# Performance work log

Measured on AMD Instinct MI355X. Metric: run time of the kernel, lower is better.

## Reference

```python
import jax, jax.numpy as jnp
import numpy as np

V, E, H, S, B = 32000, 512, 512, 512, 32  # vocab, emb=n_unit, hidden, srclen, batch


def _lstm_zero_state_step(x, W_ih, b_ih, b_hh):
    """PyTorch LSTM single step with zero initial (h, c).
    With h0 = 0, the recurrent term h0 @ W_hh^T vanishes, so W_hh does not
    affect the output (faithful to the original, which never passes state).
    Gate order i, f, g, o. Works on [..., in_dim] batched inputs.
    """
    gates = x @ W_ih.T + b_ih + b_hh
    i, f, g, o = jnp.split(gates, 4, axis=-1)
    c = jax.nn.sigmoid(i) * jnp.tanh(g)  # f gate multiplies c0 = 0
    h = jax.nn.sigmoid(o) * jnp.tanh(c)
    return h, c


def setup_inputs() -> dict:
    key = jax.random.key(0)
    ks = jax.random.split(key, 10)
    s = 1.0 / np.sqrt(H)
    return {
        "src_seqs": jax.random.randint(ks[0], (S, B), 0, V),
        "W_emb": jax.random.normal(ks[1], (V, E), dtype=jnp.float32) * 0.02,
        # read LSTM (E -> H)
        "W_ih_r": jax.random.uniform(ks[2], (4 * H, E), minval=-s, maxval=s),
        "b_ih_r": jax.random.uniform(ks[3], (4 * H,), minval=-s, maxval=s),
        "b_hh_r": jax.random.uniform(ks[4], (4 * H,), minval=-s, maxval=s),
        # compose MLP (2H -> 2H)
        "W_c": jax.random.uniform(ks[5], (2 * H, 2 * H), minval=-s, maxval=s),
        "b_c": jax.random.uniform(ks[6], (2 * H,), minval=-s, maxval=s),
        # write LSTM (2H -> H)
        "W_ih_w": jax.random.uniform(ks[7], (4 * H, 2 * H), minval=-s, maxval=s),
        "b_ih_w": jax.random.uniform(ks[8], (4 * H,), minval=-s, maxval=s),
        "b_hh_w": jax.random.uniform(ks[9], (4 * H,), minval=-s, maxval=s),
    }


def reference(src_seqs, W_emb, W_ih_r, b_ih_r, b_hh_r, W_c, b_c,
              W_ih_w, b_ih_w, b_hh_w):
    emb = W_emb[src_seqs]                     # [S, B, E]
    # read LSTM is stateless per step (zero init state each call) -> vectorize
    o_all, _ = _lstm_zero_state_step(emb, W_ih_r, b_ih_r, b_hh_r)  # [S, B, H]
    M0 = jnp.transpose(emb, (1, 0, 2))        # [B, S, H] memory

    def step(M, o_t):
        # read: attention over memory
        z = jax.nn.softmax(jnp.einsum('bsh,bh->bs', M, o_t), axis=1)  # [B, S]
        m = jnp.einsum('bs,bsh->bh', z, M)                            # [B, H]
        # compose
        c_in = jnp.concatenate([o_t, m], axis=1) @ W_c.T + b_c        # [B, 2H]
        # write LSTM (also stateless per call)
        h, cell = _lstm_zero_state_step(c_in, W_ih_w, b_ih_w, b_hh_w)  # [B, H]
        # erase/write memory update
        M_new = (1.0 - z)[..., None] * M + z[..., None] * h[:, None, :]
        return M_new, (h, cell)

    _, (hs, cells) = jax.lax.scan(step, M0, o_all)
    outputs = hs                              # [S, B, H]
    h_n = hs[-1][None]                        # [1, B, H] (n_layer=1)
    c_n = cells[-1][None]                     # [1, B, H]
    return outputs, h_n, c_n
```

## Files before the change

### kernel.cpp

```cpp
#include <hip/hip_runtime.h>
#include <hip/hip_bf16.h>

#define S_LEN 512
#define B_SZ  32
#define H_DIM 512
#define KC    1024

typedef __attribute__((ext_vector_type(8)))  short  short8;
typedef __attribute__((ext_vector_type(4)))  float  f32x4;
typedef __attribute__((ext_vector_type(2)))  float  f32x2;

static __device__ __forceinline__ unsigned short f2bf(float f){
  unsigned u = __float_as_uint(f);
  u += 0x7fffu + ((u >> 16) & 1u);
  return (unsigned short)(u >> 16);
}
static __device__ __forceinline__ short8 cvt8(float4 a, float4 b){
  short8 r;
  r[0]=(short)f2bf(a.x); r[1]=(short)f2bf(a.y); r[2]=(short)f2bf(a.z); r[3]=(short)f2bf(a.w);
  r[4]=(short)f2bf(b.x); r[5]=(short)f2bf(b.y); r[6]=(short)f2bf(b.z); r[7]=(short)f2bf(b.w);
  return r;
}
static __device__ __forceinline__ short8 cvt8e(f32x4 a, f32x4 b){
  short8 r;
  r[0]=(short)f2bf(a[0]); r[1]=(short)f2bf(a[1]); r[2]=(short)f2bf(a[2]); r[3]=(short)f2bf(a[3]);
  r[4]=(short)f2bf(b[0]); r[5]=(short)f2bf(b[1]); r[6]=(short)f2bf(b[2]); r[7]=(short)f2bf(b[3]);
  return r;
}
static __device__ __forceinline__ float sigf(float x){ return 1.0f/(1.0f+__expf(-x)); }
static __device__ __forceinline__ float tanh_(float x){
  float e = __expf(2.0f*x);
  return (e-1.0f)/(e+1.0f);
}

static __device__ __forceinline__ void st_ag(float* p, float v){
  __hip_atomic_store(p, v, __ATOMIC_RELAXED, __HIP_MEMORY_SCOPE_AGENT);
}
static __device__ __forceinline__ f32x2 ld2_ag(const float* p){
  unsigned long long u = __hip_atomic_load((unsigned long long*)p, __ATOMIC_RELAXED, __HIP_MEMORY_SCOPE_AGENT);
  f32x2 r; r[0] = __uint_as_float((unsigned)u); r[1] = __uint_as_float((unsigned)(u>>32));
  return r;
}

__global__ __launch_bounds__(256) void k_gather_emb(const int* __restrict__ src,
    const float* __restrict__ Wemb, unsigned short* __restrict__ embB){
  int gid = blockIdx.x*256 + threadIdx.x;
  int row = gid >> 6;
  int k   = (gid & 63) * 8;
  int idx = src[row];
  const float* p = Wemb + (size_t)idx*H_DIM + k;
  float4 a = *(const float4*)p;
  float4 b = *(const float4*)(p+4);
  *(short8*)(embB + (size_t)gid*8) = cvt8(a,b);
}

__global__ __launch_bounds__(256) void k_perm_wr(const float* __restrict__ W,
    unsigned short* __restrict__ out){
  int gid = blockIdx.x*256 + threadIdx.x;
  int n = gid >> 6;
  int k = (gid & 63)*8;
  int j = (n&3)*512 + (n>>2);
  const float* p = W + (size_t)j*512 + k;
  float4 a = *(const float4*)p;
  float4 b = *(const float4*)(p+4);
  *(short8*)(out + (size_t)gid*8) = cvt8(a,b);
}

__global__ __launch_bounds__(256) void k_perm_wihw(const float* __restrict__ W,
    unsigned short* __restrict__ out){
  int gid = blockIdx.x*256 + threadIdx.x;
  int n = gid >> 7;
  int k = (gid & 127)*8;
  int j = (n&3)*512 + (n>>2);
  const float* p = W + (size_t)j*KC + k;
  float4 a = *(const float4*)p;
  float4 b = *(const float4*)(p+4);
  *(short8*)(out + (size_t)gid*8) = cvt8(a,b);
}

__global__ __launch_bounds__(256) void k_wcT(const float* __restrict__ Wc,
    unsigned short* __restrict__ out){
  __shared__ float tile[64][65];
  int bx = blockIdx.x & 15, by = blockIdx.x >> 4;
  int c0 = bx*64, r0 = by*64;
  int row = threadIdx.x >> 2;
  int cp  = (threadIdx.x & 3)*16;
  for (int i=0;i<16;i+=4){
    float4 v = *(const float4*)&Wc[(size_t)(r0+row)*KC + c0 + cp + i];
    tile[row][cp+i+0]=v.x; tile[row][cp+i+1]=v.y; tile[row][cp+i+2]=v.z; tile[row][cp+i+3]=v.w;
  }
  __syncthreads();
  short8 s0, s1;
  for(int i=0;i<8;++i){
    s0[i]=(short)f2bf(tile[cp+i][row]);
    s1[i]=(short)f2bf(tile[cp+8+i][row]);
  }
  unsigned short* op = out + (size_t)(c0+row)*KC + r0 + cp;
  *(short8*)op = s0; *(short8*)(op+8) = s1;
}

__global__ __launch_bounds__(256) void k_bias_r(const float* __restrict__ bi,
    const float* __restrict__ bh, float* __restrict__ out){
  int n = blockIdx.x*256 + threadIdx.x;
  int j = (n&3)*512 + (n>>2);
  out[n] = bi[j] + bh[j];
}

__global__ __launch_bounds__(256) void k_bcomb(const float* __restrict__ Wihw,
    const float* __restrict__ bc, const float* __restrict__ bi,
    const float* __restrict__ bh, float* __restrict__ out){
  int n = blockIdx.x*256 + threadIdx.x;
  int j = (n&3)*512 + (n>>2);
  const float* wp = Wihw + (size_t)j*KC;
  float s = 0.f;
  for (int l=0;l<KC;l+=4){
    float4 w = *(const float4*)&wp[l];
    float4 c = *(const float4*)&bc[l];
    s += w.x*c.x + w.y*c.y + w.z*c.z + w.w*c.w;
  }
  out[n] = s + bi[j] + bh[j];
}

template<int EPI>
__global__ __launch_bounds__(256) void gemm_k(const unsigned short* __restrict__ A,
    const unsigned short* __restrict__ Bm, int K, int bnCnt,
    const float* __restrict__ bias, float* __restrict__ outF,
    unsigned short* __restrict__ outB, int outStride){
  __shared__ __align__(16) char smem[66560];
  unsigned short* As = (unsigned short*)smem;
  unsigned short* Bs = As + 128*72;
  float* epi = (float*)smem;
  const int tid = threadIdx.x, lane = tid & 63, w = tid >> 6;
  const int wr = w >> 1, wc = w & 1;
  const int bm = blockIdx.x / bnCnt, bn = blockIdx.x % bnCnt;
  f32x4 acc[4][4] = {};
  const size_t Abase = (size_t)bm*128*K;
  const size_t Bbase = (size_t)bn*128*K;
  for (int k0 = 0; k0 < K; k0 += 64){
    __syncthreads();
    #pragma unroll
    for (int i = 0; i < 4; ++i){
      int idx = tid + i*256;
      int row = idx >> 3, cb = (idx & 7)*8;
      *(short8*)&As[row*72 + cb] = *(const short8*)&A[Abase + (size_t)row*K + k0 + cb];
      *(short8*)&Bs[row*72 + cb] = *(const short8*)&Bm[Bbase + (size_t)row*K + k0 + cb];
    }
    __syncthreads();
    #pragma unroll
    for (int kk = 0; kk < 64; kk += 32){
      short8 af[4], bf[4];
      #pragma unroll
      for (int i=0;i<4;++i) af[i] = *(short8*)&As[(wr*64 + i*16 + (lane&15))*72 + kk + (lane>>4)*8];
      #pragma unroll
      for (int j=0;j<4;++j) bf[j] = *(short8*)&Bs[(wc*64 + j*16 + (lane&15))*72 + kk + (lane>>4)*8];
      #pragma unroll
      for (int i=0;i<4;++i)
        #pragma unroll
        for (int j=0;j<4;++j)
          acc[i][j] = __builtin_amdgcn_mfma_f32_16x16x32_bf16(af[i], bf[j], acc[i][j], 0,0,0);
    }
  }
  if (EPI == 0){
    float bj[4];
    #pragma unroll
    for (int j=0;j<4;++j) bj[j] = bias[bn*128 + wc*64 + j*16 + (lane&15)];
    __syncthreads();
    float* ep = epi + w*(64*65);
    #pragma unroll
    for (int i=0;i<4;++i)
      #pragma unroll
      for (int j=0;j<4;++j)
        #pragma unroll
        for (int r=0;r<4;++r)
          ep[(i*16 + (lane>>4)*4 + r)*65 + j*16 + (lane&15)] = acc[i][j][r] + bj[j];
    __syncthreads();
    int rg = bm*128 + wr*64 + lane;
    #pragma unroll
    for (int q=0;q<16;++q){
      float gi = ep[lane*65 + q*4+0];
      float gg = ep[lane*65 + q*4+2];
      float go = ep[lane*65 + q*4+3];
      float c = sigf(gi)*tanh_(gg);
      float h = sigf(go)*tanh_(c);
      outF[(size_t)rg*H_DIM + bn*32 + wc*16 + q] = h;
    }
  } else {
    #pragma unroll
    for (int i=0;i<4;++i)
      #pragma unroll
      for (int j=0;j<4;++j)
        #pragma unroll
        for (int r=0;r<4;++r){
          int rg = bm*128 + wr*64 + i*16 + (lane>>4)*4 + r;
          int cg = bn*128 + wc*64 + j*16 + (lane&15);
          outB[(size_t)rg*outStride + cg] = f2bf(acc[i][j][r]);
        }
  }
}

static __device__ __forceinline__ void gbar(int* cnt, int tid, int target){
  __syncthreads();
  asm volatile("s_waitcnt vmcnt(0)" ::: "memory");
  if (tid == 0){
    __hip_atomic_fetch_add(cnt, 1, __ATOMIC_RELAXED, __HIP_MEMORY_SCOPE_AGENT);
    while (__hip_atomic_load(cnt, __ATOMIC_RELAXED, __HIP_MEMORY_SCOPE_AGENT) < target)
      __builtin_amdgcn_s_sleep(1);
  }
  __syncthreads();
  asm volatile("" ::: "memory");
}

static __device__ __forceinline__ float blockReduce(float v, bool isMax, float* red4, int lane, int wv){
  #pragma unroll
  for (int m=32;m>0;m>>=1){
    float o = __shfl_xor(v, m);
    v = isMax ? fmaxf(v,o) : v+o;
  }
  __syncthreads();
  if (lane==0) red4[wv] = v;
  __syncthreads();
  float r0=red4[0], r1=red4[1], r2=red4[2], r3=red4[3];
  return isMax ? fmaxf(fmaxf(r0,r1),fmaxf(r2,r3)) : (r0+r1)+(r2+r3);
}

__global__ __launch_bounds__(256,1) void scan_k(
    const int* __restrict__ src, const float* __restrict__ Wemb,
    const float* __restrict__ o_all, const unsigned short* __restrict__ Wcomb,
    const float* __restrict__ bcomb,
    float* __restrict__ dbuf, float* __restrict__ mglob,
    float* __restrict__ hbuf, float* __restrict__ out,
    int* __restrict__ cnts){
  __shared__ __align__(16) float Mrow[64*512];
  __shared__ __align__(16) char ubuf[8256];
  __shared__ __align__(16) float gates[4][68];
  __shared__ float z_lds[512];
  __shared__ float red4[4];
  __shared__ float zt_own[64], zp_own[64];

  const int tid = threadIdx.x, lane = tid & 63, wv = tid >> 6;
  const int bid = blockIdx.x;
  const int g = bid & 7, s = bid >> 3;
  const int b = g*4 + (s & 3), chunk = s >> 2;
  const int cbase = chunk*64;
  const int n0 = s*64;
  int* bcnt = cnts + g*64;
  const int cA = lane*4, cB = 256 + lane*4;

  if (tid < 64){
    st_ag(&mglob[((size_t)0*B_SZ + b)*H_DIM + cbase + tid], 0.f);
    st_ag(&mglob[((size_t)1*B_SZ + b)*H_DIM + cbase + tid], 0.f);
    st_ag(&hbuf[((size_t)1*B_SZ + b)*H_DIM + cbase + tid], 0.f);
  }
  z_lds[tid] = 0.f; z_lds[tid+256] = 0.f;
  {
    const float* o0 = o_all + (size_t)b*H_DIM;
    f32x4 osA = *(const f32x4*)&o0[cA];
    f32x4 osB = *(const f32x4*)&o0[cB];
    for (int rr=0; rr<16; ++rr){
      int lr = wv*16 + rr;
      int sgl = cbase + lr;
      int idx = src[sgl*B_SZ + b];
      const float* wp = Wemb + (size_t)idx*H_DIM;
      f32x4 v0 = *(const f32x4*)&wp[cA];
      f32x4 v1 = *(const f32x4*)&wp[cB];
      *(f32x4*)&Mrow[lr*512 + cA] = v0;
      *(f32x4*)&Mrow[lr*512 + cB] = v1;
      float dd = v0[0]*osA[0]+v0[1]*osA[1]+v0[2]*osA[2]+v0[3]*osA[3]
               + v1[0]*osB[0]+v1[1]*osB[1]+v1[2]*osB[2]+v1[3]*osB[3];
      #pragma unroll
      for (int m=32;m>0;m>>=1) dd += __shfl_xor(dd, m);
      if (lane==0) st_ag(&dbuf[(size_t)b*S_LEN + sgl], dd);
    }
  }
  int tgt = 32;
  gbar(bcnt, tid, tgt); tgt += 32;

  for (int t=0; t<S_LEN; ++t){
    const int pw = t & 1, po = pw ^ 1;
    const float* dR = dbuf + ((size_t)pw*B_SZ + b)*S_LEN;
    float* dW = dbuf + ((size_t)po*B_SZ + b)*S_LEN;
    const float* hR = hbuf + ((size_t)po*B_SZ + b)*H_DIM;
    const float* ot = o_all + ((size_t)t*B_SZ + b)*H_DIM;

    if (tid < 64) st_ag(&mglob[((size_t)po*B_SZ + b)*H_DIM + cbase + tid], 0.f);

    f32x2 d2  = ld2_ag(&dR[2*tid]);
    f32x2 hp2 = ld2_ag(&hR[2*tid]);
    f32x2 a0 = ld2_ag(&hR[cA]), a1 = ld2_ag(&hR[cA+2]);
    f32x2 b0 = ld2_ag(&hR[cB]), b1 = ld2_ag(&hR[cB+2]);
    f32x4 hA4 = (f32x4){a0[0],a0[1],a1[0],a1[1]};
    f32x4 hB4 = (f32x4){b0[0],b0[1],b1[0],b1[1]};

    f32x2 ot2 = *(const f32x2*)&ot[2*tid];
    float hd = blockReduce(hp2[0]*ot2[0] + hp2[1]*ot2[1], false, red4, lane, wv);

    float zp0 = z_lds[2*tid], zp1 = z_lds[2*tid+1];
    float sc0 = (1.f - zp0)*d2[0] + zp0*hd;
    float sc1 = (1.f - zp1)*d2[1] + zp1*hd;
    float mx = blockReduce(fmaxf(sc0,sc1), true, red4, lane, wv);
    float ex0 = __expf(sc0 - mx), ex1 = __expf(sc1 - mx);
    float sm = blockReduce(ex0+ex1, false, red4, lane, wv);
    float inv = 1.f / sm;
    float zt0 = ex0*inv, zt1 = ex1*inv;
    z_lds[2*tid] = zt0; z_lds[2*tid+1] = zt1;
    {
      unsigned r = (unsigned)(2*tid) - (unsigned)cbase;
      if (r < 64u){ zt_own[r] = zt0; zp_own[r] = zp0; zt_own[r+1] = zt1; zp_own[r+1] = zp1; }
    }
    __syncthreads();

    const bool hasNext = (t < S_LEN-1);
    const float* onx = o_all + ((size_t)(hasNext? t+1 : t)*B_SZ + b)*H_DIM;
    f32x4 osA = *(const f32x4*)&onx[cA];
    f32x4 osB = *(const f32x4*)&onx[cB];
    float m0=0,m1=0,m2=0,m3=0,m4=0,m5=0,m6=0,m7=0;
    for (int rr=0; rr<16; ++rr){
      int lr = wv*16 + rr;
      float zp = zp_own[lr], zt = zt_own[lr];
      float* mpA = &Mrow[lr*512 + cA];
      float* mpB = &Mrow[lr*512 + cB];
      f32x4 v0 = *(f32x4*)mpA;
      f32x4 v1 = *(f32x4*)mpB;
      v0[0] += zp*(hA4[0]-v0[0]); v0[1] += zp*(hA4[1]-v0[1]);
      v0[2] += zp*(hA4[2]-v0[2]); v0[3] += zp*(hA4[3]-v0[3]);
      v1[0] += zp*(hB4[0]-v1[0]); v1[1] += zp*(hB4[1]-v1[1]);
      v1[2] += zp*(hB4[2]-v1[2]); v1[3] += zp*(hB4[3]-v1[3]);
      *(f32x4*)mpA = v0; *(f32x4*)mpB = v1;
      m0 += zt*v0[0]; m1 += zt*v0[1]; m2 += zt*v0[2]; m3 += zt*v0[3];
      m4 += zt*v1[0]; m5 += zt*v1[1]; m6 += zt*v1[2]; m7 += zt*v1[3];
      float dd = v0[0]*osA[0]+v0[1]*osA[1]+v0[2]*osA[2]+v0[3]*osA[3]
               + v1[0]*osB[0]+v1[1]*osB[1]+v1[2]*osB[2]+v1[3]*osB[3];
      #pragma unroll
      for (int m=32;m>0;m>>=1) dd += __shfl_xor(dd, m);
      if (lane==0 && hasNext) st_ag(&dW[cbase + lr], dd);
    }
    __syncthreads();
    {
      float* mst = (float*)ubuf;
      *(f32x4*)&mst[wv*512 + cA] = (f32x4){m0,m1,m2,m3};
      *(f32x4*)&mst[wv*512 + cB] = (f32x4){m4,m5,m6,m7};
      __syncthreads();
      int i0 = tid*2;
      float s0v = mst[i0]   + mst[512+i0]   + mst[1024+i0]   + mst[1536+i0];
      float s1v = mst[i0+1] + mst[512+i0+1] + mst[1024+i0+1] + mst[1536+i0+1];
      float* mg = mglob + ((size_t)pw*B_SZ + b)*H_DIM;
      atomicAdd(&mg[i0],   s0v);
      atomicAdd(&mg[i0+1], s1v);
    }
    gbar(bcnt, tid, tgt); tgt += 32;

    {
      unsigned short* xl = (unsigned short*)ubuf;
      {
        const int q = wv, idx = lane*8;
        const int gb = g*4 + q;
        const float* oB = o_all + ((size_t)t*B_SZ + gb)*H_DIM;
        f32x4 o0 = *(const f32x4*)&oB[idx];
        f32x4 o1 = *(const f32x4*)&oB[idx+4];
        *(short8*)&xl[q*1032 + idx] = cvt8e(o0,o1);
        const float* mg = mglob + ((size_t)pw*B_SZ + gb)*H_DIM;
        f32x2 q0 = ld2_ag(mg+idx),   q1 = ld2_ag(mg+idx+2);
        f32x2 q2 = ld2_ag(mg+idx+4), q3 = ld2_ag(mg+idx+6);
        f32x4 f0 = (f32x4){q0[0],q0[1],q1[0],q1[1]};
        f32x4 f1 = (f32x4){q2[0],q2[1],q3[0],q3[1]};
        *(short8*)&xl[q*1032 + 512 + idx] = cvt8e(f0,f1);
      }
      __syncthreads();
      {
        const int r15 = lane & 15, q8 = (lane>>4)*8;
        const unsigned short* wp = Wcomb + (size_t)(n0 + wv*16 + r15)*KC;
        f32x4 acc = {0,0,0,0};
        #pragma unroll
        for (int kt=0; kt<32; ++kt){
          int k = kt*32 + q8;
          short8 af = *(const short8*)&xl[(r15&3)*1032 + k];
          short8 bf = *(const short8*)&wp[k];
          acc = __builtin_amdgcn_mfma_f32_16x16x32_bf16(af, bf, acc, 0,0,0);
        }
        if (lane < 16){
          #pragma unroll
          for (int r=0;r<4;++r) gates[r][wv*16 + r15] = acc[r];
        }
      }
      __syncthreads();
      if (tid < 64){
        int q = tid >> 4, p = tid & 15;
        int gb = g*4 + q;
        int hq = s*16 + p;
        float g4[4];
        #pragma unroll
        for (int gg2=0; gg2<4; ++gg2)
          g4[gg2] = gates[q][p*4+gg2] + bcomb[n0 + p*4+gg2];
        float ccv = sigf(g4[0])*tanh_(g4[2]);
        float hh  = sigf(g4[3])*tanh_(ccv);
        st_ag(&hbuf[((size_t)pw*B_SZ + gb)*H_DIM + hq], hh);
        out[((size_t)t*B_SZ + gb)*H_DIM + hq] = hh;
        if (t == S_LEN-1){
          out[(size_t)S_LEN*B_SZ*H_DIM + (size_t)gb*H_DIM + hq] = hh;
          out[(size_t)S_LEN*B_SZ*H_DIM + (size_t)B_SZ*H_DIM + (size_t)gb*H_DIM + hq] = ccv;
        }
      }
    }
    gbar(bcnt, tid, tgt); tgt += 32;
  }
}

extern "C" void kernel_launch(void* const* d_in, const int* in_sizes, int n_in,
                              void* d_out, int out_size, void* d_ws, size_t ws_size,
                              hipStream_t stream){
  const int*   src   = (const int*)  d_in[0];
  const float* Wemb  = (const float*)d_in[1];
  const float* Wihr  = (const float*)d_in[2];
  const float* bihr  = (const float*)d_in[3];
  const float* bhhr  = (const float*)d_in[4];
  const float* Wc    = (const float*)d_in[5];
  const float* bc    = (const float*)d_in[6];
  const float* Wihw  = (const float*)d_in[7];
  const float* bihw  = (const float*)d_in[8];
  const float* bhhw  = (const float*)d_in[9];
  float* out = (float*)d_out;

  char* ws = (char*)d_ws;
  size_t off = 0;
  auto alloc = [&](size_t bytes)->char*{
    char* p = ws + off; off += (bytes + 255) & ~(size_t)255; return p;
  };
  unsigned short* embB  = (unsigned short*)alloc((size_t)16384*512*2);
  float*          o_all = (float*)         alloc((size_t)16384*512*4);
  unsigned short* WrP   = (unsigned short*)alloc((size_t)2048*512*2);
  unsigned short* WiwP  = (unsigned short*)alloc((size_t)2048*1024*2);
  unsigned short* WcT   = (unsigned short*)alloc((size_t)1024*1024*2);
  unsigned short* Wcomb = (unsigned short*)alloc((size_t)2048*1024*2);
  float*          bperm = (float*)alloc(2048*4);
  float*          bcomb = (float*)alloc(2048*4);
  float*          dbuf  = (float*)alloc((size_t)2*32*512*4);
  float*          mglob = (float*)alloc((size_t)2*32*512*4);
  float*          hbuf  = (float*)alloc((size_t)2*32*512*4);
  int*            cnts  = (int*)  alloc(4096);

  hipMemsetAsync(cnts, 0, 4096, stream);
  k_gather_emb<<<4096,256,0,stream>>>(src, Wemb, embB);
  k_perm_wr  <<<512, 256,0,stream>>>(Wihr, WrP);
  k_perm_wihw<<<1024,256,0,stream>>>(Wihw, WiwP);
  k_wcT      <<<256, 256,0,stream>>>(Wc, WcT);
  k_bias_r   <<<8,   256,0,stream>>>(bihr, bhhr, bperm);
  k_bcomb    <<<8,   256,0,stream>>>(Wihw, bc, bihw, bhhw, bcomb);
  gemm_k<0><<<2048,256,0,stream>>>(embB, WrP, 512, 16, bperm, o_all, nullptr, 0);
  gemm_k<1><<<128,256,0,stream>>>(WiwP, WcT, 1024, 8, nullptr, nullptr, Wcomb, 1024);
  scan_k<<<256,256,0,stream>>>(src, Wemb, o_all, Wcomb, bcomb,
                               dbuf, mglob, hbuf, out, cnts);
}
```

Before: 7.618 ms.

## Precompute o-part of compose gates via GEMM and split scan by hidden columns

The scan kernel is reorganized so each block owns one batch element and a 64-column slice of memory across all sequence positions, keeping its M slice and its slice of the Wcomb m-half weights in registers. The o_t contribution to the write-LSTM gates is precomputed for all timesteps with a new GEMM and stored as int16 fixed-point, so per step only the m_t part (K=512) is computed. Partial attention scores and partial gates are exchanged across the 8 column blocks of a batch through two per-batch counter barriers. This trades the old cross-batch-group sync and atomicAdd reductions for more global partial-sum traffic, a large extra gatesO buffer, and a quantization risk from the fixed-point scale and clamp.

```diff
diff --git a/kernel.cpp b/kernel.cpp
--- a/kernel.cpp
+++ b/kernel.cpp
@@ -21,12 +21,6 @@
   r[4]=(short)f2bf(b.x); r[5]=(short)f2bf(b.y); r[6]=(short)f2bf(b.z); r[7]=(short)f2bf(b.w);
   return r;
 }
-static __device__ __forceinline__ short8 cvt8e(f32x4 a, f32x4 b){
-  short8 r;
-  r[0]=(short)f2bf(a[0]); r[1]=(short)f2bf(a[1]); r[2]=(short)f2bf(a[2]); r[3]=(short)f2bf(a[3]);
-  r[4]=(short)f2bf(b[0]); r[5]=(short)f2bf(b[1]); r[6]=(short)f2bf(b[2]); r[7]=(short)f2bf(b[3]);
-  return r;
-}
 static __device__ __forceinline__ float sigf(float x){ return 1.0f/(1.0f+__expf(-x)); }
 static __device__ __forceinline__ float tanh_(float x){
   float e = __expf(2.0f*x);
@@ -36,10 +30,8 @@
 static __device__ __forceinline__ void st_ag(float* p, float v){
   __hip_atomic_store(p, v, __ATOMIC_RELAXED, __HIP_MEMORY_SCOPE_AGENT);
 }
-static __device__ __forceinline__ f32x2 ld2_ag(const float* p){
-  unsigned long long u = __hip_atomic_load((unsigned long long*)p, __ATOMIC_RELAXED, __HIP_MEMORY_SCOPE_AGENT);
-  f32x2 r; r[0] = __uint_as_float((unsigned)u); r[1] = __uint_as_float((unsigned)(u>>32));
-  return r;
+static __device__ __forceinline__ float ld_ag(const float* p){
+  return __hip_atomic_load((float*)p, __ATOMIC_RELAXED, __HIP_MEMORY_SCOPE_AGENT);
 }
 
 __global__ __launch_bounds__(256) void k_gather_emb(const int* __restrict__ src,
@@ -123,9 +115,9 @@
 
 template<int EPI>
 __global__ __launch_bounds__(256) void gemm_k(const unsigned short* __restrict__ A,
-    const unsigned short* __restrict__ Bm, int K, int bnCnt,
+    const unsigned short* __restrict__ Bm, int K, int bStride, int bnCnt,
     const float* __restrict__ bias, float* __restrict__ outF,
-    unsigned short* __restrict__ outB, int outStride){
+    unsigned short* __restrict__ outB, short* __restrict__ outI, int outStride){
   __shared__ __align__(16) char smem[66560];
   unsigned short* As = (unsigned short*)smem;
   unsigned short* Bs = As + 128*72;
@@ -135,7 +127,7 @@
   const int bm = blockIdx.x / bnCnt, bn = blockIdx.x % bnCnt;
   f32x4 acc[4][4] = {};
   const size_t Abase = (size_t)bm*128*K;
-  const size_t Bbase = (size_t)bn*128*K;
+  const size_t Bbase = (size_t)bn*128*bStride;
   for (int k0 = 0; k0 < K; k0 += 64){
     __syncthreads();
     #pragma unroll
@@ -143,7 +135,7 @@
       int idx = tid + i*256;
       int row = idx >> 3, cb = (idx & 7)*8;
       *(short8*)&As[row*72 + cb] = *(const short8*)&A[Abase + (size_t)row*K + k0 + cb];
-      *(short8*)&Bs[row*72 + cb] = *(const short8*)&Bm[Bbase + (size_t)row*K + k0 + cb];
+      *(short8*)&Bs[row*72 + cb] = *(const short8*)&Bm[Bbase + (size_t)row*bStride + k0 + cb];
     }
     __syncthreads();
     #pragma unroll
@@ -182,9 +174,11 @@
       float go = ep[lane*65 + q*4+3];
       float c = sigf(gi)*tanh_(gg);
       float h = sigf(go)*tanh_(c);
-      outF[(size_t)rg*H_DIM + bn*32 + wc*16 + q] = h;
-    }
-  } else {
+      int cg = bn*32 + wc*16 + q;
+      outF[(size_t)rg*H_DIM + cg] = h;
+      outB[(size_t)rg*H_DIM + cg] = f2bf(h);
+    }
+  } else if (EPI == 1){
     #pragma unroll
     for (int i=0;i<4;++i)
       #pragma unroll
@@ -195,213 +189,209 @@
           int cg = bn*128 + wc*64 + j*16 + (lane&15);
           outB[(size_t)rg*outStride + cg] = f2bf(acc[i][j][r]);
         }
-  }
-}
-
-static __device__ __forceinline__ void gbar(int* cnt, int tid, int target){
-  __syncthreads();
-  asm volatile("s_waitcnt vmcnt(0)" ::: "memory");
-  if (tid == 0){
-    __hip_atomic_fetch_add(cnt, 1, __ATOMIC_RELAXED, __HIP_MEMORY_SCOPE_AGENT);
-    while (__hip_atomic_load(cnt, __ATOMIC_RELAXED, __HIP_MEMORY_SCOPE_AGENT) < target)
-      __builtin_amdgcn_s_sleep(1);
-  }
-  __syncthreads();
-  asm volatile("" ::: "memory");
-}
-
-static __device__ __forceinline__ float blockReduce(float v, bool isMax, float* red4, int lane, int wv){
-  #pragma unroll
-  for (int m=32;m>0;m>>=1){
-    float o = __shfl_xor(v, m);
-    v = isMax ? fmaxf(v,o) : v+o;
-  }
-  __syncthreads();
-  if (lane==0) red4[wv] = v;
-  __syncthreads();
-  float r0=red4[0], r1=red4[1], r2=red4[2], r3=red4[3];
-  return isMax ? fmaxf(fmaxf(r0,r1),fmaxf(r2,r3)) : (r0+r1)+(r2+r3);
+  } else {
+    #pragma unroll
+    for (int i=0;i<4;++i)
+      #pragma unroll
+      for (int j=0;j<4;++j)
+        #pragma unroll
+        for (int r=0;r<4;++r){
+          int rg = bm*128 + wr*64 + i*16 + (lane>>4)*4 + r;
+          int cg = bn*128 + wc*64 + j*16 + (lane&15);
+          float v = acc[i][j][r] * 4096.0f;
+          v = fminf(fmaxf(v, -32767.0f), 32767.0f);
+          outI[(size_t)rg*outStride + cg] = (short)__float2int_rn(v);
+        }
+  }
 }
 
 __global__ __launch_bounds__(256,1) void scan_k(
     const int* __restrict__ src, const float* __restrict__ Wemb,
     const float* __restrict__ o_all, const unsigned short* __restrict__ Wcomb,
-    const float* __restrict__ bcomb,
-    float* __restrict__ dbuf, float* __restrict__ mglob,
-    float* __restrict__ hbuf, float* __restrict__ out,
-    int* __restrict__ cnts){
-  __shared__ __align__(16) float Mrow[64*512];
-  __shared__ __align__(16) char ubuf[8256];
-  __shared__ __align__(16) float gates[4][68];
+    const float* __restrict__ bcomb, const short* __restrict__ gatesO,
+    float* __restrict__ dpart, float* __restrict__ gpart,
+    float* __restrict__ out, int* __restrict__ cnts){
+  __shared__ __align__(16) float M[512*66];
   __shared__ float z_lds[512];
+  __shared__ float o_lds[64];
+  __shared__ float h_lds[64];
+  __shared__ float m_lds[64];
+  __shared__ float part4[256];
+  __shared__ float gg[256];
   __shared__ float red4[4];
-  __shared__ float zt_own[64], zp_own[64];
 
   const int tid = threadIdx.x, lane = tid & 63, wv = tid >> 6;
   const int bid = blockIdx.x;
-  const int g = bid & 7, s = bid >> 3;
-  const int b = g*4 + (s & 3), chunk = s >> 2;
-  const int cbase = chunk*64;
-  const int n0 = s*64;
-  int* bcnt = cnts + g*64;
-  const int cA = lane*4, cB = 256 + lane*4;
-
-  if (tid < 64){
-    st_ag(&mglob[((size_t)0*B_SZ + b)*H_DIM + cbase + tid], 0.f);
-    st_ag(&mglob[((size_t)1*B_SZ + b)*H_DIM + cbase + tid], 0.f);
-    st_ag(&hbuf[((size_t)1*B_SZ + b)*H_DIM + cbase + tid], 0.f);
-  }
+  const int c = bid & 7, b = bid >> 3;
+  int* dcnt = cnts + b*64;
+  int* gcnt = cnts + 2048 + b*64;
+  float* dslot = dpart + ((size_t)b*8 + c)*512;
+  float* gslot = gpart + ((size_t)b*8 + c)*2048;
+
+  short8 wf[64];
+  {
+    const unsigned short* wbase = Wcomb + 512 + c*64 + (lane>>4)*8;
+    #pragma unroll
+    for (int i=0;i<32;++i){
+      int n = (wv*32 + i)*16 + (lane&15);
+      const unsigned short* wp = wbase + (size_t)n*KC;
+      wf[i*2+0] = *(const short8*)(wp);
+      wf[i*2+1] = *(const short8*)(wp + 32);
+    }
+  }
+
+  if (tid < 64){ h_lds[tid] = 0.f; }
   z_lds[tid] = 0.f; z_lds[tid+256] = 0.f;
-  {
-    const float* o0 = o_all + (size_t)b*H_DIM;
-    f32x4 osA = *(const f32x4*)&o0[cA];
-    f32x4 osB = *(const f32x4*)&o0[cB];
-    for (int rr=0; rr<16; ++rr){
-      int lr = wv*16 + rr;
-      int sgl = cbase + lr;
-      int idx = src[sgl*B_SZ + b];
-      const float* wp = Wemb + (size_t)idx*H_DIM;
-      f32x4 v0 = *(const f32x4*)&wp[cA];
-      f32x4 v1 = *(const f32x4*)&wp[cB];
-      *(f32x4*)&Mrow[lr*512 + cA] = v0;
-      *(f32x4*)&Mrow[lr*512 + cB] = v1;
-      float dd = v0[0]*osA[0]+v0[1]*osA[1]+v0[2]*osA[2]+v0[3]*osA[3]
-               + v1[0]*osB[0]+v1[1]*osB[1]+v1[2]*osB[2]+v1[3]*osB[3];
-      #pragma unroll
-      for (int m=32;m>0;m>>=1) dd += __shfl_xor(dd, m);
-      if (lane==0) st_ag(&dbuf[(size_t)b*S_LEN + sgl], dd);
-    }
-  }
-  int tgt = 32;
-  gbar(bcnt, tid, tgt); tgt += 32;
+  #pragma unroll
+  for (int r=0;r<2;++r){
+    int s = tid + r*256;
+    int idx = src[s*B_SZ + b];
+    const float* wp = Wemb + (size_t)idx*H_DIM + c*64;
+    float* mp = &M[s*66];
+    #pragma unroll
+    for (int k=0;k<64;k+=4){
+      float4 v = *(const float4*)&wp[k];
+      *(f32x2*)&mp[k]   = (f32x2){v.x, v.y};
+      *(f32x2*)&mp[k+2] = (f32x2){v.z, v.w};
+    }
+  }
+  __syncthreads();
 
   for (int t=0; t<S_LEN; ++t){
-    const int pw = t & 1, po = pw ^ 1;
-    const float* dR = dbuf + ((size_t)pw*B_SZ + b)*S_LEN;
-    float* dW = dbuf + ((size_t)po*B_SZ + b)*S_LEN;
-    const float* hR = hbuf + ((size_t)po*B_SZ + b)*H_DIM;
-    const float* ot = o_all + ((size_t)t*B_SZ + b)*H_DIM;
-
-    if (tid < 64) st_ag(&mglob[((size_t)po*B_SZ + b)*H_DIM + cbase + tid], 0.f);
-
-    f32x2 d2  = ld2_ag(&dR[2*tid]);
-    f32x2 hp2 = ld2_ag(&hR[2*tid]);
-    f32x2 a0 = ld2_ag(&hR[cA]), a1 = ld2_ag(&hR[cA+2]);
-    f32x2 b0 = ld2_ag(&hR[cB]), b1 = ld2_ag(&hR[cB+2]);
-    f32x4 hA4 = (f32x4){a0[0],a0[1],a1[0],a1[1]};
-    f32x4 hB4 = (f32x4){b0[0],b0[1],b1[0],b1[1]};
-
-    f32x2 ot2 = *(const f32x2*)&ot[2*tid];
-    float hd = blockReduce(hp2[0]*ot2[0] + hp2[1]*ot2[1], false, red4, lane, wv);
-
-    float zp0 = z_lds[2*tid], zp1 = z_lds[2*tid+1];
-    float sc0 = (1.f - zp0)*d2[0] + zp0*hd;
-    float sc1 = (1.f - zp1)*d2[1] + zp1*hd;
-    float mx = blockReduce(fmaxf(sc0,sc1), true, red4, lane, wv);
+    if (tid < 64) o_lds[tid] = o_all[((size_t)t*B_SZ + b)*H_DIM + c*64 + tid];
+    __syncthreads();
+
+    #pragma unroll
+    for (int r=0;r<2;++r){
+      int s = tid + r*256;
+      float zp = z_lds[s];
+      float* mp = &M[s*66];
+      float dd = 0.f;
+      #pragma unroll
+      for (int k=0;k<64;k+=2){
+        f32x2 v = *(f32x2*)&mp[k];
+        f32x2 h2 = *(f32x2*)&h_lds[k];
+        f32x2 o2 = *(f32x2*)&o_lds[k];
+        v[0] += zp*(h2[0]-v[0]); v[1] += zp*(h2[1]-v[1]);
+        *(f32x2*)&mp[k] = v;
+        dd += v[0]*o2[0] + v[1]*o2[1];
+      }
+      st_ag(&dslot[s], dd);
+    }
+
+    __syncthreads();
+    asm volatile("s_waitcnt vmcnt(0)" ::: "memory");
+    if (tid == 0){
+      __hip_atomic_fetch_add(dcnt, 1, __ATOMIC_RELAXED, __HIP_MEMORY_SCOPE_AGENT);
+      int tg = 8*(t+1);
+      while (__hip_atomic_load(dcnt, __ATOMIC_RELAXED, __HIP_MEMORY_SCOPE_AGENT) < tg)
+        __builtin_amdgcn_s_sleep(1);
+    }
+    __syncthreads();
+    asm volatile("" ::: "memory");
+
+    float sc0 = 0.f, sc1 = 0.f;
+    #pragma unroll
+    for (int c2=0;c2<8;++c2){
+      const float* dp = dpart + ((size_t)b*8 + c2)*512;
+      sc0 += ld_ag(&dp[tid]);
+      sc1 += ld_ag(&dp[tid+256]);
+    }
+    float mx, sm;
+    {
+      float v = fmaxf(sc0, sc1);
+      #pragma unroll
+      for (int m2=32;m2>0;m2>>=1) v = fmaxf(v, __shfl_xor(v, m2));
+      __syncthreads();
+      if (lane==0) red4[wv] = v;
+      __syncthreads();
+      mx = fmaxf(fmaxf(red4[0],red4[1]), fmaxf(red4[2],red4[3]));
+    }
     float ex0 = __expf(sc0 - mx), ex1 = __expf(sc1 - mx);
-    float sm = blockReduce(ex0+ex1, false, red4, lane, wv);
+    {
+      float v = ex0 + ex1;
+      #pragma unroll
+      for (int m2=32;m2>0;m2>>=1) v += __shfl_xor(v, m2);
+      __syncthreads();
+      if (lane==0) red4[wv] = v;
+      __syncthreads();
+      sm = (red4[0]+red4[1]) + (red4[2]+red4[3]);
+    }
     float inv = 1.f / sm;
-    float zt0 = ex0*inv, zt1 = ex1*inv;
-    z_lds[2*tid] = zt0; z_lds[2*tid+1] = zt1;
+    z_lds[tid] = ex0*inv;
+    z_lds[tid+256] = ex1*inv;
+    __syncthreads();
+
     {
-      unsigned r = (unsigned)(2*tid) - (unsigned)cbase;
-      if (r < 64u){ zt_own[r] = zt0; zp_own[r] = zp0; zt_own[r+1] = zt1; zp_own[r+1] = zp1; }
-    }
-    __syncthreads();
-
-    const bool hasNext = (t < S_LEN-1);
-    const float* onx = o_all + ((size_t)(hasNext? t+1 : t)*B_SZ + b)*H_DIM;
-    f32x4 osA = *(const f32x4*)&onx[cA];
-    f32x4 osB = *(const f32x4*)&onx[cB];
-    float m0=0,m1=0,m2=0,m3=0,m4=0,m5=0,m6=0,m7=0;
-    for (int rr=0; rr<16; ++rr){
-      int lr = wv*16 + rr;
-      float zp = zp_own[lr], zt = zt_own[lr];
-      float* mpA = &Mrow[lr*512 + cA];
-      float* mpB = &Mrow[lr*512 + cB];
-      f32x4 v0 = *(f32x4*)mpA;
-      f32x4 v1 = *(f32x4*)mpB;
-      v0[0] += zp*(hA4[0]-v0[0]); v0[1] += zp*(hA4[1]-v0[1]);
-      v0[2] += zp*(hA4[2]-v0[2]); v0[3] += zp*(hA4[3]-v0[3]);
-      v1[0] += zp*(hB4[0]-v1[0]); v1[1] += zp*(hB4[1]-v1[1]);
-      v1[2] += zp*(hB4[2]-v1[2]); v1[3] += zp*(hB4[3]-v1[3]);
-      *(f32x4*)mpA = v0; *(f32x4*)mpB = v1;
-      m0 += zt*v0[0]; m1 += zt*v0[1]; m2 += zt*v0[2]; m3 += zt*v0[3];
-      m4 += zt*v1[0]; m5 += zt*v1[1]; m6 += zt*v1[2]; m7 += zt*v1[3];
-      float dd = v0[0]*osA[0]+v0[1]*osA[1]+v0[2]*osA[2]+v0[3]*osA[3]
-               + v1[0]*osB[0]+v1[1]*osB[1]+v1[2]*osB[2]+v1[3]*osB[3];
-      #pragma unroll
-      for (int m=32;m>0;m>>=1) dd += __shfl_xor(dd, m);
-      if (lane==0 && hasNext) st_ag(&dW[cbase + lr], dd);
-    }
-    __syncthreads();
+      int col = tid & 63;
+      int s0 = wv*128;
+      float mp = 0.f;
+      #pragma unroll 8
+      for (int s2=0;s2<128;++s2)
+        mp += z_lds[s0+s2]*M[(s0+s2)*66 + col];
+      part4[wv*64 + col] = mp;
+    }
+    __syncthreads();
+    if (tid < 64)
+      m_lds[tid] = (part4[tid]+part4[64+tid]) + (part4[128+tid]+part4[192+tid]);
+    __syncthreads();
+
     {
-      float* mst = (float*)ubuf;
-      *(f32x4*)&mst[wv*512 + cA] = (f32x4){m0,m1,m2,m3};
-      *(f32x4*)&mst[wv*512 + cB] = (f32x4){m4,m5,m6,m7};
-      __syncthreads();
-      int i0 = tid*2;
-      float s0v = mst[i0]   + mst[512+i0]   + mst[1024+i0]   + mst[1536+i0];
-      float s1v = mst[i0+1] + mst[512+i0+1] + mst[1024+i0+1] + mst[1536+i0+1];
-      float* mg = mglob + ((size_t)pw*B_SZ + b)*H_DIM;
-      atomicAdd(&mg[i0],   s0v);
-      atomicAdd(&mg[i0+1], s1v);
-    }
-    gbar(bcnt, tid, tgt); tgt += 32;
-
-    {
-      unsigned short* xl = (unsigned short*)ubuf;
-      {
-        const int q = wv, idx = lane*8;
-        const int gb = g*4 + q;
-        const float* oB = o_all + ((size_t)t*B_SZ + gb)*H_DIM;
-        f32x4 o0 = *(const f32x4*)&oB[idx];
-        f32x4 o1 = *(const f32x4*)&oB[idx+4];
-        *(short8*)&xl[q*1032 + idx] = cvt8e(o0,o1);
-        const float* mg = mglob + ((size_t)pw*B_SZ + gb)*H_DIM;
-        f32x2 q0 = ld2_ag(mg+idx),   q1 = ld2_ag(mg+idx+2);
-        f32x2 q2 = ld2_ag(mg+idx+4), q3 = ld2_ag(mg+idx+6);
-        f32x4 f0 = (f32x4){q0[0],q0[1],q1[0],q1[1]};
-        f32x4 f1 = (f32x4){q2[0],q2[1],q3[0],q3[1]};
-        *(short8*)&xl[q*1032 + 512 + idx] = cvt8e(f0,f1);
-      }
-      __syncthreads();
-      {
-        const int r15 = lane & 15, q8 = (lane>>4)*8;
-        const unsigned short* wp = Wcomb + (size_t)(n0 + wv*16 + r15)*KC;
-        f32x4 acc = {0,0,0,0};
+      short8 a0 = {0,0,0,0,0,0,0,0}, a1 = a0;
+      if ((lane & 15) == 0){
+        int kq = (lane>>4)*8;
         #pragma unroll
-        for (int kt=0; kt<32; ++kt){
-          int k = kt*32 + q8;
-          short8 af = *(const short8*)&xl[(r15&3)*1032 + k];
-          short8 bf = *(const short8*)&wp[k];
-          acc = __builtin_amdgcn_mfma_f32_16x16x32_bf16(af, bf, acc, 0,0,0);
-        }
-        if (lane < 16){
-          #pragma unroll
-          for (int r=0;r<4;++r) gates[r][wv*16 + r15] = acc[r];
+        for (int j=0;j<8;++j){
+          a0[j] = (short)f2bf(m_lds[kq+j]);
+          a1[j] = (short)f2bf(m_lds[32+kq+j]);
         }
       }
-      __syncthreads();
-      if (tid < 64){
-        int q = tid >> 4, p = tid & 15;
-        int gb = g*4 + q;
-        int hq = s*16 + p;
-        float g4[4];
-        #pragma unroll
-        for (int gg2=0; gg2<4; ++gg2)
-          g4[gg2] = gates[q][p*4+gg2] + bcomb[n0 + p*4+gg2];
-        float ccv = sigf(g4[0])*tanh_(g4[2]);
-        float hh  = sigf(g4[3])*tanh_(ccv);
-        st_ag(&hbuf[((size_t)pw*B_SZ + gb)*H_DIM + hq], hh);
-        out[((size_t)t*B_SZ + gb)*H_DIM + hq] = hh;
-        if (t == S_LEN-1){
-          out[(size_t)S_LEN*B_SZ*H_DIM + (size_t)gb*H_DIM + hq] = hh;
-          out[(size_t)S_LEN*B_SZ*H_DIM + (size_t)B_SZ*H_DIM + (size_t)gb*H_DIM + hq] = ccv;
-        }
+      #pragma unroll
+      for (int i=0;i<32;++i){
+        f32x4 acc = {0.f,0.f,0.f,0.f};
+        acc = __builtin_amdgcn_mfma_f32_16x16x32_bf16(a0, wf[i*2+0], acc, 0,0,0);
+        acc = __builtin_amdgcn_mfma_f32_16x16x32_bf16(a1, wf[i*2+1], acc, 0,0,0);
+        if (lane < 16)
+          st_ag(&gslot[wv*512 + i*16 + lane], acc[0]);
       }
     }
-    gbar(bcnt, tid, tgt); tgt += 32;
+
+    __syncthreads();
+    asm volatile("s_waitcnt vmcnt(0)" ::: "memory");
+    if (tid == 0){
+      __hip_atomic_fetch_add(gcnt, 1, __ATOMIC_RELAXED, __HIP_MEMORY_SCOPE_AGENT);
+      int tg = 8*(t+1);
+      while (__hip_atomic_load(gcnt, __ATOMIC_RELAXED, __HIP_MEMORY_SCOPE_AGENT) < tg)
+        __builtin_amdgcn_s_sleep(1);
+    }
+    __syncthreads();
+    asm volatile("" ::: "memory");
+
+    {
+      int col = c*256 + tid;
+      float gv = bcomb[col]
+               + (float)gatesO[((size_t)t*B_SZ + b)*2048 + col] * (1.0f/4096.0f);
+      #pragma unroll
+      for (int c2=0;c2<8;++c2)
+        gv += ld_ag(&gpart[((size_t)b*8 + c2)*2048 + col]);
+      gg[tid] = gv;
+    }
+    __syncthreads();
+    if (tid < 64){
+      float gi = gg[tid*4+0];
+      float gG = gg[tid*4+2];
+      float go = gg[tid*4+3];
+      float ccv = sigf(gi)*tanh_(gG);
+      float hh  = sigf(go)*tanh_(ccv);
+      h_lds[tid] = hh;
+      int hq = c*64 + tid;
+      out[((size_t)t*B_SZ + b)*H_DIM + hq] = hh;
+      if (t == S_LEN-1){
+        out[(size_t)S_LEN*B_SZ*H_DIM + (size_t)b*H_DIM + hq] = hh;
+        out[(size_t)S_LEN*B_SZ*H_DIM + (size_t)B_SZ*H_DIM + (size_t)b*H_DIM + hq] = ccv;
+      }
+    }
+    __syncthreads();
   }
 }
 
@@ -427,26 +417,28 @@
   };
   unsigned short* embB  = (unsigned short*)alloc((size_t)16384*512*2);
   float*          o_all = (float*)         alloc((size_t)16384*512*4);
+  unsigned short* o_allB= (unsigned short*)alloc((size_t)16384*512*2);
   unsigned short* WrP   = (unsigned short*)alloc((size_t)2048*512*2);
   unsigned short* WiwP  = (unsigned short*)alloc((size_t)2048*1024*2);
   unsigned short* WcT   = (unsigned short*)alloc((size_t)1024*1024*2);
   unsigned short* Wcomb = (unsigned short*)alloc((size_t)2048*1024*2);
   float*          bperm = (float*)alloc(2048*4);
   float*          bcomb = (float*)alloc(2048*4);
-  float*          dbuf  = (float*)alloc((size_t)2*32*512*4);
-  float*          mglob = (float*)alloc((size_t)2*32*512*4);
-  float*          hbuf  = (float*)alloc((size_t)2*32*512*4);
-  int*            cnts  = (int*)  alloc(4096);
-
-  hipMemsetAsync(cnts, 0, 4096, stream);
+  short*          gatesO= (short*)alloc((size_t)16384*2048*2);
+  float*          dpart = (float*)alloc((size_t)32*8*512*4);
+  float*          gpart = (float*)alloc((size_t)32*8*2048*4);
+  int*            cnts  = (int*)  alloc(16384);
+
+  hipMemsetAsync(cnts, 0, 16384, stream);
   k_gather_emb<<<4096,256,0,stream>>>(src, Wemb, embB);
   k_perm_wr  <<<512, 256,0,stream>>>(Wihr, WrP);
   k_perm_wihw<<<1024,256,0,stream>>>(Wihw, WiwP);
   k_wcT      <<<256, 256,0,stream>>>(Wc, WcT);
   k_bias_r   <<<8,   256,0,stream>>>(bihr, bhhr, bperm);
   k_bcomb    <<<8,   256,0,stream>>>(Wihw, bc, bihw, bhhw, bcomb);
-  gemm_k<0><<<2048,256,0,stream>>>(embB, WrP, 512, 16, bperm, o_all, nullptr, 0);
-  gemm_k<1><<<128,256,0,stream>>>(WiwP, WcT, 1024, 8, nullptr, nullptr, Wcomb, 1024);
-  scan_k<<<256,256,0,stream>>>(src, Wemb, o_all, Wcomb, bcomb,
-                               dbuf, mglob, hbuf, out, cnts);
-}
+  gemm_k<0><<<2048,256,0,stream>>>(embB, WrP, 512, 512, 16, bperm, o_all, o_allB, nullptr, H_DIM);
+  gemm_k<1><<<128,256,0,stream>>>(WiwP, WcT, 1024, 1024, 8, nullptr, nullptr, Wcomb, nullptr, 1024);
+  gemm_k<2><<<2048,256,0,stream>>>(o_allB, Wcomb, 512, 1024, 16, nullptr, nullptr, nullptr, gatesO, 2048);
+  scan_k<<<256,256,0,stream>>>(src, Wemb, o_all, Wcomb, bcomb, gatesO,
+                               dpart, gpart, out, cnts);
+}
```

Result: slower. 8.197 ms (+7.6%).
